# Performance work log

Hardware: AMD Instinct MI355X
Metric: run time of the kernel (lower is better)

## Reference

```python
import jax, jax.numpy as jnp
import numpy as np

CONF_THRES = 0.8   # from module constant
NMS_THRES = 0.4    # from module constant
PERSON_ID = 0      # COCO 'person' is class index 0 in coco.names
IMG_SIZE = 416.0
TOPK = 4096        # static cap on post-threshold candidates (>= expected survivors)


def setup_inputs() -> dict:
    key = jax.random.key(0)
    B, N, C = 8, 10647, 85  # YOLOv3@416: (13^2+26^2+52^2)*3 anchors, 4+1+80 channels
    det = jax.random.uniform(key, (B, N, C), dtype=jnp.float32)
    # scale xywh columns to pixel coordinates; obj/class confs stay in [0,1]
    scale = jnp.concatenate([jnp.full((4,), IMG_SIZE, jnp.float32),
                             jnp.ones((C - 4,), jnp.float32)])
    return {"detections": det * scale}


def _xywh2xyxy(b):
    x, y, w, h = b[..., 0], b[..., 1], b[..., 2], b[..., 3]
    return jnp.stack([x - w / 2, y - h / 2, x + w / 2, y + h / 2], axis=-1)


def _iou_matrix(boxes):
    # boxes [K,4] xyxy; matches torch-yolov3 bbox_iou (+1 pixel convention, 1e-16 eps)
    x1, y1, x2, y2 = boxes[:, 0], boxes[:, 1], boxes[:, 2], boxes[:, 3]
    iw = jnp.clip(jnp.minimum(x2[:, None], x2[None, :]) - jnp.maximum(x1[:, None], x1[None, :]) + 1, 0)
    ih = jnp.clip(jnp.minimum(y2[:, None], y2[None, :]) - jnp.maximum(y1[:, None], y1[None, :]) + 1, 0)
    inter = iw * ih
    area = (x2 - x1 + 1) * (y2 - y1 + 1)
    return inter / (area[:, None] + area[None, :] - inter + 1e-16)


def _nms_image(det):
    # det [N,85]: greedy class-aware NMS identical in keep-set to the torch loop
    obj = det[:, 4]
    cls_conf = jnp.max(det[:, 5:], axis=-1)
    cls_pred = jnp.argmax(det[:, 5:], axis=-1)
    valid = obj >= CONF_THRES
    # torch sorts candidates by obj_conf * max class conf, descending
    score = jnp.where(valid, obj * cls_conf, -jnp.inf)
    _, idx = jax.lax.top_k(score, TOPK)
    boxes = _xywh2xyxy(det[idx, :4])
    cc = cls_conf[idx]
    cp = cls_pred[idx]
    v = valid[idx]
    overlap = (_iou_matrix(boxes) > NMS_THRES) & (cp[:, None] == cp[None, :])
    upper = jnp.arange(TOPK)[None, :] > jnp.arange(TOPK)[:, None]  # only suppress later boxes

    def body(i, supp):
        alive = (~supp[i]) & v[i]
        return supp | (overlap[i] & upper[i] & alive)

    supp = jax.lax.fori_loop(0, TOPK, body, jnp.zeros((TOPK,), bool))
    keep = v & ~supp
    # _extract_results: class-conf probs sorted descending per image
    probs = jnp.where(keep, cc, 0.0)
    probs = jnp.flip(jnp.sort(probs), axis=-1)
    # image contributes only if 'person' detected (CATEGORY_NAME check)
    is_ok = jnp.any(keep & (cp == PERSON_ID))
    return probs * is_ok.astype(probs.dtype)


def reference(detections):
    # [B, TOPK] padded prob matrix; rows without a kept 'person' box are zeroed
    return jax.vmap(_nms_image)(detections)
```

## Files before the change

### kernel.cpp

```cpp
#include <hip/hip_runtime.h>


#define NCH    85
#define NCLS   80
#define TOPK   4096
#define CAP    96
#define KBLK   64
#define RWAVES 8

__device__ __forceinline__ float rlf(float v, int l) {
    return __uint_as_float(__builtin_amdgcn_readlane(__float_as_uint(v), l));
}
__device__ __forceinline__ int rli(int v, int l) {
    return __builtin_amdgcn_readlane(v, l);
}

__global__ void score_kernel(const float* __restrict__ det,
                             float2* __restrict__ A,
                             unsigned char* __restrict__ Cc,
                             float4* __restrict__ REC,
                             int N, int NP, int total) {
#pragma clang fp contract(off)
    int w    = (blockIdx.x * blockDim.x + threadIdx.x) >> 6;
    int lane = threadIdx.x & 63;
    if (w >= total) return;
    const float* row = det + (size_t)w * NCH;
    int b = w / N, i = w - b * N;

    float obj = row[4];
    if (obj < 0.8f) {
        if (lane == 0) Cc[(size_t)b * NP + i] = 0xFFu;
        return;
    }
    float va = row[lane];
    float vb = (lane < NCH - 64) ? row[64 + lane] : -1.0f;
    float bestv = -1.0f; int bestc = 1 << 30;
    if (lane >= 5) { bestv = va; bestc = lane - 5; }
    if (lane < NCH - 64) {
        int c2 = 59 + lane;
        if (vb > bestv || (vb == bestv && c2 < bestc)) { bestv = vb; bestc = c2; }
    }
    for (int m = 32; m >= 1; m >>= 1) {
        float ov = __shfl_xor(bestv, m);
        int   oc = __shfl_xor(bestc, m);
        if (ov > bestv || (ov == bestv && oc < bestc)) { bestv = ov; bestc = oc; }
    }
    float x  = rlf(va, 0), y  = rlf(va, 1);
    float bw = rlf(va, 2), bh = rlf(va, 3);
    if (lane == 0) {
        float hw = bw * 0.5f, hh = bh * 0.5f;
        A[(size_t)b * NP + i]  = make_float2(obj * bestv, bestv);
        Cc[(size_t)b * NP + i] = (unsigned char)bestc;
        REC[(size_t)w] = make_float4(x - hw, y - hh, x + hw, y + hh);
    }
}

__global__ void __launch_bounds__(64) nms_kernel(
        const float2* __restrict__ A,
        const unsigned char* __restrict__ Cc,
        const float4* __restrict__ REC,
        float* __restrict__ kv,
        int*   __restrict__ kcnt,
        int N, int NT, int NP) {
#pragma clang fp contract(off)
    int cell = blockIdx.x;
    int b = cell / NCLS, c = cell % NCLS;
    int lane = threadIdx.x;
    unsigned long long mlt = (1ull << lane) - 1ull;

    __shared__ int lidx[CAP];
    __shared__ int tmpidx[CAP];

    const unsigned char* Cb = Cc + (size_t)b * NP;
    int cnt = 0;
    uint4 q = *(const uint4*)(Cb + lane * 16);
    for (int t = 0; t < NT; t++) {
        uint4 qn;
        if (t + 1 < NT) qn = *(const uint4*)(Cb + (size_t)(t + 1) * 1024 + lane * 16);
        int i0 = t * 1024 + lane * 16;
        unsigned xs[4] = { q.x, q.y, q.z, q.w };
        unsigned mm = 0;
        #pragma unroll
        for (int kk = 0; kk < 16; kk++) {
            unsigned byte = (xs[kk >> 2] >> ((kk & 3) * 8)) & 0xFFu;
            if (byte == (unsigned)c && (i0 + kk) < N) mm |= 1u << kk;
        }
        if (__ballot(mm != 0)) {
            #pragma unroll
            for (int kk = 0; kk < 16; kk++) {
                unsigned long long mk = __ballot((mm >> kk) & 1u);
                if (mk) {
                    if ((mm >> kk) & 1u) {
                        int p = cnt + __popcll(mk & mlt);
                        if (p < CAP) lidx[p] = i0 + kk;
                    }
                    cnt += __popcll(mk);
                }
            }
        }
        q = qn;
    }
    int n = cnt < CAP ? cnt : CAP;
    if (n == 0) { if (lane == 0) kcnt[cell] = 0; return; }

    bool a0 = lane < n, a1 = lane + 64 < n;
    const float2* Ab = A + (size_t)b * NP;
    int id0 = a0 ? lidx[lane]      : 0;
    int id1 = a1 ? lidx[lane + 64] : 0;
    float s0 = a0 ? Ab[id0].x : 0.0f;
    float s1 = a1 ? Ab[id1].x : 0.0f;

    int r0 = 0, r1 = 0;
    int m0 = n < 64 ? n : 64;
    for (int j = 0; j < m0; j++) {
        float sj = rlf(s0, j); int ij = rli(id0, j);
        r0 += (sj > s0) || (sj == s0 && ij < id0);
        r1 += (sj > s1) || (sj == s1 && ij < id1);
    }
    for (int j = 64; j < n; j++) {
        float sj = rlf(s1, j - 64); int ij = rli(id1, j - 64);
        r0 += (sj > s0) || (sj == s0 && ij < id0);
        r1 += (sj > s1) || (sj == s1 && ij < id1);
    }
    if (a0) tmpidx[r0] = id0;
    if (a1) tmpidx[r1] = id1;
    int di0 = a0 ? tmpidx[lane]      : 0;
    int di1 = a1 ? tmpidx[lane + 64] : 0;

    float scc = 0, x10 = 0, y10 = 0, x20 = 0, y20 = 0, ar0 = 0;
    if (a0) {
        scc = Ab[di0].y;
        float4 rc = REC[(size_t)b * N + di0];
        x10 = rc.x; y10 = rc.y; x20 = rc.z; y20 = rc.w;
        ar0 = (x20 - x10 + 1.0f) * (y20 - y10 + 1.0f);
    }
    float tcc = 0, x11 = 0, y11 = 0, x21 = 0, y21 = 0, ar1 = 0;
    if (a1) {
        tcc = Ab[di1].y;
        float4 rc = REC[(size_t)b * N + di1];
        x11 = rc.x; y11 = rc.y; x21 = rc.z; y21 = rc.w;
        ar1 = (x21 - x11 + 1.0f) * (y21 - y11 + 1.0f);
    }

    unsigned long long col0 = 0, col1a = 0, col1b = 0;
    for (int i = 0; i < n; i++) {
        float ix1, iy1, ix2, iy2, iar;
        if (i < 64) {
            ix1 = rlf(x10, i); iy1 = rlf(y10, i);
            ix2 = rlf(x20, i); iy2 = rlf(y20, i); iar = rlf(ar0, i);
        } else {
            ix1 = rlf(x11, i - 64); iy1 = rlf(y11, i - 64);
            ix2 = rlf(x21, i - 64); iy2 = rlf(y21, i - 64); iar = rlf(ar1, i - 64);
        }
        if (lane > i && lane < n) {
            float iw = fminf(ix2, x20) - fmaxf(ix1, x10) + 1.0f;
            float ih = fminf(iy2, y20) - fmaxf(iy1, y10) + 1.0f;
            iw = fmaxf(iw, 0.0f); ih = fmaxf(ih, 0.0f);
            float inter = iw * ih;
            float iou = inter / (iar + ar0 - inter + 1e-16f);
            if (iou > 0.4f) col0 |= 1ull << i;
        }
        if (n > 64) {
            int j2 = lane + 64;
            if (j2 > i && j2 < n) {
                float iw = fminf(ix2, x21) - fmaxf(ix1, x11) + 1.0f;
                float ih = fminf(iy2, y21) - fmaxf(iy1, y11) + 1.0f;
                iw = fmaxf(iw, 0.0f); ih = fmaxf(ih, 0.0f);
                float inter = iw * ih;
                float iou = inter / (iar + ar1 - inter + 1e-16f);
                if (iou > 0.4f) {
                    if (i < 64) col1a |= 1ull << i;
                    else        col1b |= 1ull << (i - 64);
                }
            }
        }
    }

    bool sup0 = false, sup1 = false;
    for (int ii = 0; ii < n; ii++) {
        bool alive;
        if (ii < 64) alive = !((__ballot(sup0) >> ii) & 1ull);
        else         alive = !((__ballot(sup1) >> (ii - 64)) & 1ull);
        if (alive) {
            if (ii < 64) {
                sup0 = sup0 | (((col0  >> ii) & 1ull) != 0);
                sup1 = sup1 | (((col1a >> ii) & 1ull) != 0);
            } else {
                sup1 = sup1 | (((col1b >> (ii - 64)) & 1ull) != 0);
            }
        }
    }

    unsigned long long alive0 = __ballot((!sup0) && a0);
    int kn0 = __popcll(alive0);
    unsigned long long alive1 = (n > 64) ? __ballot((!sup1) && a1) : 0ull;
    int kn = kn0 + __popcll(alive1);
    float* kvc = kv + (size_t)cell * CAP;
    if ((!sup0) && a0) kvc[__popcll(alive0 & mlt)] = scc;
    if ((!sup1) && a1) kvc[kn0 + __popcll(alive1 & mlt)] = tcc;
    if (lane == 0) kcnt[cell] = kn;
}

__global__ void __launch_bounds__(512) rank_out_kernel(
        const float* __restrict__ kv,
        const int*   __restrict__ kcnt,
        float* __restrict__ out) {
    int b     = blockIdx.x / KBLK;
    int chunk = blockIdx.x % KBLK;
    int tid   = threadIdx.x;
    int lane  = tid & 63;
    int wid   = tid >> 6;
    int i     = chunk * 64 + lane;

    __shared__ int   off[NCLS];
    __shared__ float v[TOPK] __attribute__((aligned(16)));
    __shared__ int   part[RWAVES][64];

    if (tid < NCLS) off[tid] = kcnt[b * NCLS + tid];
    __syncthreads();
    #pragma unroll
    for (int s = 1; s < NCLS; s <<= 1) {
        int x = 0;
        if (tid < NCLS && tid >= s) x = off[tid - s];
        __syncthreads();
        if (tid < NCLS) off[tid] += x;
        __syncthreads();
    }
    int cnt = off[NCLS - 1];
    if (cnt > TOPK) cnt = TOPK;
    float f = (off[0] > 0) ? 1.0f : 0.0f;

    if (chunk * 64 >= cnt) {
        if (wid == 0) out[(size_t)b * TOPK + i] = 0.0f;
        return;
    }

    for (int cell = wid; cell < NCLS; cell += RWAVES) {
        int e1 = off[cell];
        int e0 = (cell == 0) ? 0 : off[cell - 1];
        int kc = e1 - e0;
        const float* src = kv + (size_t)(b * NCLS + cell) * CAP;
        for (int j = lane; j < kc; j += 64)
            if (e0 + j < TOPK) v[e0 + j] = src[j];
    }
    __syncthreads();

    float val = (i < cnt) ? v[i] : 0.0f;
    int seg = (cnt + RWAVES - 1) / RWAVES;
    int j0 = wid * seg;
    int j1 = j0 + seg; if (j1 > cnt) j1 = cnt;

    int r = 0, j = j0;
    for (; j < j1 && (j & 3); j++) {
        float t = v[j]; r += (t > val) || (t == val && j < i);
    }
    for (; j + 4 <= j1; j += 4) {
        float4 q = *(const float4*)&v[j];
        r += (q.x > val) || (q.x == val && (j + 0) < i);
        r += (q.y > val) || (q.y == val && (j + 1) < i);
        r += (q.z > val) || (q.z == val && (j + 2) < i);
        r += (q.w > val) || (q.w == val && (j + 3) < i);
    }
    for (; j < j1; j++) {
        float t = v[j]; r += (t > val) || (t == val && j < i);
    }
    part[wid][lane] = r;
    __syncthreads();

    if (wid == 0) {
        if (i < cnt) {
            int rank = 0;
            #pragma unroll
            for (int qq = 0; qq < RWAVES; qq++) rank += part[qq][lane];
            out[(size_t)b * TOPK + rank] = val * f;
        } else {
            out[(size_t)b * TOPK + i] = 0.0f;
        }
    }
}

extern "C" void kernel_launch(void* const* d_in, const int* in_sizes, int n_in,
                              void* d_out, int out_size, void* d_ws, size_t ws_size,
                              hipStream_t stream) {
    const float* det = (const float*)d_in[0];
    float* out = (float*)d_out;

    int B = out_size / TOPK;
    int N = in_sizes[0] / (B * NCH);
    int total = B * N;
    int NT = (N + 1023) / 1024;
    int NP = NT * 1024;

    char* p = (char*)d_ws;
    auto align256 = [](size_t x) { return (x + 255) & ~(size_t)255; };
    size_t o = 0;
    unsigned char* Cc = (unsigned char*)(p + o); o = align256(o + (size_t)B * NP);
    float2* A   = (float2*)(p + o);              o = align256(o + (size_t)B * NP * sizeof(float2));
    float4* REC = (float4*)(p + o);              o = align256(o + (size_t)total * sizeof(float4));
    float*  kv  = (float*)(p + o);               o = align256(o + (size_t)B * NCLS * CAP * sizeof(float));
    int*   kcnt = (int*)(p + o);

    int gridA = (total + 3) / 4;
    score_kernel<<<gridA, 256, 0, stream>>>(det, A, Cc, REC, N, NP, total);
    nms_kernel<<<B * NCLS, 64, 0, stream>>>(A, Cc, REC, kv, kcnt, N, NT, NP);
    rank_out_kernel<<<B * KBLK, 512, 0, stream>>>(kv, kcnt, out);
}
```

Baseline: 62.18 us.

## Fuse NMS and rank-output kernels via per-image atomic completion counters

Result: slower. 115.0 us (+85.0%).

```diff
diff --git a/kernel.cpp b/kernel.cpp
--- a/kernel.cpp
+++ b/kernel.cpp
@@ -7,6 +7,8 @@
 #define CAP    96
 #define KBLK   64
 #define RWAVES 8
+#define PBB    80
+#define BPI    10
 
 __device__ __forceinline__ float rlf(float v, int l) {
     return __uint_as_float(__builtin_amdgcn_readlane(__float_as_uint(v), l));
@@ -19,8 +21,11 @@
                              float2* __restrict__ A,
                              unsigned char* __restrict__ Cc,
                              float4* __restrict__ REC,
+                             int* __restrict__ done,
                              int N, int NP, int total) {
 #pragma clang fp contract(off)
+    if (blockIdx.x == 0 && threadIdx.x < 16) done[threadIdx.x] = 0;
+
     int w    = (blockIdx.x * blockDim.x + threadIdx.x) >> 6;
     int lane = threadIdx.x & 63;
     if (w >= total) return;
@@ -55,166 +60,178 @@
     }
 }
 
-__global__ void __launch_bounds__(64) nms_kernel(
+__global__ void __launch_bounds__(512, 4) fused_kernel(
         const float2* __restrict__ A,
         const unsigned char* __restrict__ Cc,
         const float4* __restrict__ REC,
         float* __restrict__ kv,
         int*   __restrict__ kcnt,
+        int*   __restrict__ done,
+        float* __restrict__ out,
         int N, int NT, int NP) {
 #pragma clang fp contract(off)
-    int cell = blockIdx.x;
-    int b = cell / NCLS, c = cell % NCLS;
-    int lane = threadIdx.x;
-    unsigned long long mlt = (1ull << lane) - 1ull;
-
-    __shared__ int lidx[CAP];
-    __shared__ int tmpidx[CAP];
-
-    const unsigned char* Cb = Cc + (size_t)b * NP;
-    int cnt = 0;
-    uint4 q = *(const uint4*)(Cb + lane * 16);
-    for (int t = 0; t < NT; t++) {
-        uint4 qn;
-        if (t + 1 < NT) qn = *(const uint4*)(Cb + (size_t)(t + 1) * 1024 + lane * 16);
-        int i0 = t * 1024 + lane * 16;
-        unsigned xs[4] = { q.x, q.y, q.z, q.w };
-        unsigned mm = 0;
-        #pragma unroll
-        for (int kk = 0; kk < 16; kk++) {
-            unsigned byte = (xs[kk >> 2] >> ((kk & 3) * 8)) & 0xFFu;
-            if (byte == (unsigned)c && (i0 + kk) < N) mm |= 1u << kk;
-        }
-        if (__ballot(mm != 0)) {
-            #pragma unroll
-            for (int kk = 0; kk < 16; kk++) {
-                unsigned long long mk = __ballot((mm >> kk) & 1u);
-                if (mk) {
-                    if ((mm >> kk) & 1u) {
-                        int p = cnt + __popcll(mk & mlt);
-                        if (p < CAP) lidx[p] = i0 + kk;
-                    }
-                    cnt += __popcll(mk);
-                }
-            }
-        }
-        q = qn;
-    }
-    int n = cnt < CAP ? cnt : CAP;
-    if (n == 0) { if (lane == 0) kcnt[cell] = 0; return; }
-
-    bool a0 = lane < n, a1 = lane + 64 < n;
-    const float2* Ab = A + (size_t)b * NP;
-    int id0 = a0 ? lidx[lane]      : 0;
-    int id1 = a1 ? lidx[lane + 64] : 0;
-    float s0 = a0 ? Ab[id0].x : 0.0f;
-    float s1 = a1 ? Ab[id1].x : 0.0f;
-
-    int r0 = 0, r1 = 0;
-    int m0 = n < 64 ? n : 64;
-    for (int j = 0; j < m0; j++) {
-        float sj = rlf(s0, j); int ij = rli(id0, j);
-        r0 += (sj > s0) || (sj == s0 && ij < id0);
-        r1 += (sj > s1) || (sj == s1 && ij < id1);
-    }
-    for (int j = 64; j < n; j++) {
-        float sj = rlf(s1, j - 64); int ij = rli(id1, j - 64);
-        r0 += (sj > s0) || (sj == s0 && ij < id0);
-        r1 += (sj > s1) || (sj == s1 && ij < id1);
-    }
-    if (a0) tmpidx[r0] = id0;
-    if (a1) tmpidx[r1] = id1;
-    int di0 = a0 ? tmpidx[lane]      : 0;
-    int di1 = a1 ? tmpidx[lane + 64] : 0;
-
-    float scc = 0, x10 = 0, y10 = 0, x20 = 0, y20 = 0, ar0 = 0;
-    if (a0) {
-        scc = Ab[di0].y;
-        float4 rc = REC[(size_t)b * N + di0];
-        x10 = rc.x; y10 = rc.y; x20 = rc.z; y20 = rc.w;
-        ar0 = (x20 - x10 + 1.0f) * (y20 - y10 + 1.0f);
-    }
-    float tcc = 0, x11 = 0, y11 = 0, x21 = 0, y21 = 0, ar1 = 0;
-    if (a1) {
-        tcc = Ab[di1].y;
-        float4 rc = REC[(size_t)b * N + di1];
-        x11 = rc.x; y11 = rc.y; x21 = rc.z; y21 = rc.w;
-        ar1 = (x21 - x11 + 1.0f) * (y21 - y11 + 1.0f);
-    }
-
-    unsigned long long col0 = 0, col1a = 0, col1b = 0;
-    for (int i = 0; i < n; i++) {
-        float ix1, iy1, ix2, iy2, iar;
-        if (i < 64) {
-            ix1 = rlf(x10, i); iy1 = rlf(y10, i);
-            ix2 = rlf(x20, i); iy2 = rlf(y20, i); iar = rlf(ar0, i);
-        } else {
-            ix1 = rlf(x11, i - 64); iy1 = rlf(y11, i - 64);
-            ix2 = rlf(x21, i - 64); iy2 = rlf(y21, i - 64); iar = rlf(ar1, i - 64);
-        }
-        if (lane > i && lane < n) {
-            float iw = fminf(ix2, x20) - fmaxf(ix1, x10) + 1.0f;
-            float ih = fminf(iy2, y20) - fmaxf(iy1, y10) + 1.0f;
-            iw = fmaxf(iw, 0.0f); ih = fmaxf(ih, 0.0f);
-            float inter = iw * ih;
-            float iou = inter / (iar + ar0 - inter + 1e-16f);
-            if (iou > 0.4f) col0 |= 1ull << i;
-        }
-        if (n > 64) {
-            int j2 = lane + 64;
-            if (j2 > i && j2 < n) {
-                float iw = fminf(ix2, x21) - fmaxf(ix1, x11) + 1.0f;
-                float ih = fminf(iy2, y21) - fmaxf(iy1, y11) + 1.0f;
-                iw = fmaxf(iw, 0.0f); ih = fmaxf(ih, 0.0f);
-                float inter = iw * ih;
-                float iou = inter / (iar + ar1 - inter + 1e-16f);
-                if (iou > 0.4f) {
-                    if (i < 64) col1a |= 1ull << i;
-                    else        col1b |= 1ull << (i - 64);
-                }
-            }
-        }
-    }
-
-    bool sup0 = false, sup1 = false;
-    for (int ii = 0; ii < n; ii++) {
-        bool alive;
-        if (ii < 64) alive = !((__ballot(sup0) >> ii) & 1ull);
-        else         alive = !((__ballot(sup1) >> (ii - 64)) & 1ull);
-        if (alive) {
-            if (ii < 64) {
-                sup0 = sup0 | (((col0  >> ii) & 1ull) != 0);
-                sup1 = sup1 | (((col1a >> ii) & 1ull) != 0);
-            } else {
-                sup1 = sup1 | (((col1b >> (ii - 64)) & 1ull) != 0);
-            }
-        }
-    }
-
-    unsigned long long alive0 = __ballot((!sup0) && a0);
-    int kn0 = __popcll(alive0);
-    unsigned long long alive1 = (n > 64) ? __ballot((!sup1) && a1) : 0ull;
-    int kn = kn0 + __popcll(alive1);
-    float* kvc = kv + (size_t)cell * CAP;
-    if ((!sup0) && a0) kvc[__popcll(alive0 & mlt)] = scc;
-    if ((!sup1) && a1) kvc[kn0 + __popcll(alive1 & mlt)] = tcc;
-    if (lane == 0) kcnt[cell] = kn;
-}
-
-__global__ void __launch_bounds__(512) rank_out_kernel(
-        const float* __restrict__ kv,
-        const int*   __restrict__ kcnt,
-        float* __restrict__ out) {
-    int b     = blockIdx.x / KBLK;
-    int chunk = blockIdx.x % KBLK;
-    int tid   = threadIdx.x;
-    int lane  = tid & 63;
-    int wid   = tid >> 6;
-    int i     = chunk * 64 + lane;
-
+    const int bid  = blockIdx.x;
+    const int tid  = threadIdx.x;
+    const int lane = tid & 63;
+    const int wid  = tid >> 6;
+
+    __shared__ int   lidx[8][CAP];
+    __shared__ int   tmp2[8][CAP];
     __shared__ int   off[NCLS];
     __shared__ float v[TOPK] __attribute__((aligned(16)));
     __shared__ int   part[RWAVES][64];
+
+    if (bid < PBB) {
+        int cell = bid * 8 + wid;
+        int b = cell / NCLS, c = cell % NCLS;
+        unsigned long long mlt = (1ull << lane) - 1ull;
+
+        const unsigned char* Cb = Cc + (size_t)b * NP;
+        int cnt = 0;
+        uint4 q = *(const uint4*)(Cb + lane * 16);
+        for (int t = 0; t < NT; t++) {
+            uint4 qn;
+            if (t + 1 < NT) qn = *(const uint4*)(Cb + (size_t)(t + 1) * 1024 + lane * 16);
+            int i0 = t * 1024 + lane * 16;
+            unsigned xs[4] = { q.x, q.y, q.z, q.w };
+            unsigned mm = 0;
+            #pragma unroll
+            for (int kk = 0; kk < 16; kk++) {
+                unsigned byte = (xs[kk >> 2] >> ((kk & 3) * 8)) & 0xFFu;
+                if (byte == (unsigned)c && (i0 + kk) < N) mm |= 1u << kk;
+            }
+            if (__ballot(mm != 0)) {
+                #pragma unroll
+                for (int kk = 0; kk < 16; kk++) {
+                    unsigned long long mk = __ballot((mm >> kk) & 1u);
+                    if (mk) {
+                        if ((mm >> kk) & 1u) {
+                            int p = cnt + __popcll(mk & mlt);
+                            if (p < CAP) lidx[wid][p] = i0 + kk;
+                        }
+                        cnt += __popcll(mk);
+                    }
+                }
+            }
+            q = qn;
+        }
+        int n = cnt < CAP ? cnt : CAP;
+        if (n == 0) {
+            if (lane == 0) kcnt[cell] = 0;
+        } else {
+            bool a0 = lane < n, a1 = lane + 64 < n;
+            const float2* Ab = A + (size_t)b * NP;
+            int id0 = a0 ? lidx[wid][lane]      : 0;
+            int id1 = a1 ? lidx[wid][lane + 64] : 0;
+            float s0 = a0 ? Ab[id0].x : 0.0f;
+            float s1 = a1 ? Ab[id1].x : 0.0f;
+
+            int r0 = 0, r1 = 0;
+            int m0 = n < 64 ? n : 64;
+            for (int j = 0; j < m0; j++) {
+                float sj = rlf(s0, j); int ij = rli(id0, j);
+                r0 += (sj > s0) || (sj == s0 && ij < id0);
+                r1 += (sj > s1) || (sj == s1 && ij < id1);
+            }
+            for (int j = 64; j < n; j++) {
+                float sj = rlf(s1, j - 64); int ij = rli(id1, j - 64);
+                r0 += (sj > s0) || (sj == s0 && ij < id0);
+                r1 += (sj > s1) || (sj == s1 && ij < id1);
+            }
+            if (a0) tmp2[wid][r0] = id0;
+            if (a1) tmp2[wid][r1] = id1;
+            int di0 = a0 ? tmp2[wid][lane]      : 0;
+            int di1 = a1 ? tmp2[wid][lane + 64] : 0;
+
+            float scc = 0, x10 = 0, y10 = 0, x20 = 0, y20 = 0, ar0 = 0;
+            if (a0) {
+                scc = Ab[di0].y;
+                float4 rc = REC[(size_t)b * N + di0];
+                x10 = rc.x; y10 = rc.y; x20 = rc.z; y20 = rc.w;
+                ar0 = (x20 - x10 + 1.0f) * (y20 - y10 + 1.0f);
+            }
+            float tcc = 0, x11 = 0, y11 = 0, x21 = 0, y21 = 0, ar1 = 0;
+            if (a1) {
+                tcc = Ab[di1].y;
+                float4 rc = REC[(size_t)b * N + di1];
+                x11 = rc.x; y11 = rc.y; x21 = rc.z; y21 = rc.w;
+                ar1 = (x21 - x11 + 1.0f) * (y21 - y11 + 1.0f);
+            }
+
+            unsigned long long col0 = 0, col1a = 0, col1b = 0;
+            for (int i = 0; i < n; i++) {
+                float ix1, iy1, ix2, iy2, iar;
+                if (i < 64) {
+                    ix1 = rlf(x10, i); iy1 = rlf(y10, i);
+                    ix2 = rlf(x20, i); iy2 = rlf(y20, i); iar = rlf(ar0, i);
+                } else {
+                    ix1 = rlf(x11, i - 64); iy1 = rlf(y11, i - 64);
+                    ix2 = rlf(x21, i - 64); iy2 = rlf(y21, i - 64); iar = rlf(ar1, i - 64);
+                }
+                if (lane > i && lane < n) {
+                    float iw = fminf(ix2, x20) - fmaxf(ix1, x10) + 1.0f;
+                    float ih = fminf(iy2, y20) - fmaxf(iy1, y10) + 1.0f;
+                    iw = fmaxf(iw, 0.0f); ih = fmaxf(ih, 0.0f);
+                    float inter = iw * ih;
+                    float iou = inter / (iar + ar0 - inter + 1e-16f);
+                    if (iou > 0.4f) col0 |= 1ull << i;
+                }
+                if (n > 64) {
+                    int j2 = lane + 64;
+                    if (j2 > i && j2 < n) {
+                        float iw = fminf(ix2, x21) - fmaxf(ix1, x11) + 1.0f;
+                        float ih = fminf(iy2, y21) - fmaxf(iy1, y11) + 1.0f;
+                        iw = fmaxf(iw, 0.0f); ih = fmaxf(ih, 0.0f);
+                        float inter = iw * ih;
+                        float iou = inter / (iar + ar1 - inter + 1e-16f);
+                        if (iou > 0.4f) {
+                            if (i < 64) col1a |= 1ull << i;
+                            else        col1b |= 1ull << (i - 64);
+                        }
+                    }
+                }
+            }
+
+            bool sup0 = false, sup1 = false;
+            for (int ii = 0; ii < n; ii++) {
+                bool alive;
+                if (ii < 64) alive = !((__ballot(sup0) >> ii) & 1ull);
+                else         alive = !((__ballot(sup1) >> (ii - 64)) & 1ull);
+                if (alive) {
+                    if (ii < 64) {
+                        sup0 = sup0 | (((col0  >> ii) & 1ull) != 0);
+                        sup1 = sup1 | (((col1a >> ii) & 1ull) != 0);
+                    } else {
+                        sup1 = sup1 | (((col1b >> (ii - 64)) & 1ull) != 0);
+                    }
+                }
+            }
+
+            unsigned long long alive0 = __ballot((!sup0) && a0);
+            int kn0 = __popcll(alive0);
+            unsigned long long alive1 = (n > 64) ? __ballot((!sup1) && a1) : 0ull;
+            int kn = kn0 + __popcll(alive1);
+            float* kvc = kv + (size_t)cell * CAP;
+            if ((!sup0) && a0) kvc[__popcll(alive0 & mlt)] = scc;
+            if ((!sup1) && a1) kvc[kn0 + __popcll(alive1 & mlt)] = tcc;
+            if (lane == 0) kcnt[cell] = kn;
+        }
+        __syncthreads();
+        if (tid == 0)
+            __hip_atomic_fetch_add(&done[bid / BPI], 1,
+                                   __ATOMIC_RELEASE, __HIP_MEMORY_SCOPE_AGENT);
+    }
+
+    int b     = bid / KBLK;
+    int chunk = bid % KBLK;
+    int i     = chunk * 64 + lane;
+
+    if (tid == 0) {
+        while (__hip_atomic_load(&done[b], __ATOMIC_ACQUIRE,
+                                 __HIP_MEMORY_SCOPE_AGENT) < BPI)
+            __builtin_amdgcn_s_sleep(8);
+    }
+    __syncthreads();
 
     if (tid < NCLS) off[tid] = kcnt[b * NCLS + tid];
     __syncthreads();
@@ -298,10 +315,15 @@
     float2* A   = (float2*)(p + o);              o = align256(o + (size_t)B * NP * sizeof(float2));
     float4* REC = (float4*)(p + o);              o = align256(o + (size_t)total * sizeof(float4));
     float*  kv  = (float*)(p + o);               o = align256(o + (size_t)B * NCLS * CAP * sizeof(float));
-    int*   kcnt = (int*)(p + o);
+    int*   kcnt = (int*)(p + o);                 o = align256(o + (size_t)B * NCLS * sizeof(int));
+    int*   done = (int*)(p + o);
 
     int gridA = (total + 3) / 4;
-    score_kernel<<<gridA, 256, 0, stream>>>(det, A, Cc, REC, N, NP, total);
-    nms_kernel<<<B * NCLS, 64, 0, stream>>>(A, Cc, REC, kv, kcnt, N, NT, NP);
-    rank_out_kernel<<<B * KBLK, 512, 0, stream>>>(kv, kcnt, out);
-}
+    score_kernel<<<gridA, 256, 0, stream>>>(det, A, Cc, REC, done, N, NP, total);
+
+    void* args[] = { (void*)&A, (void*)&Cc, (void*)&REC, (void*)&kv,
+                     (void*)&kcnt, (void*)&done, (void*)&out,
+                     (void*)&N, (void*)&NT, (void*)&NP };
+    hipLaunchCooperativeKernel((void*)fused_kernel, dim3(B * KBLK), dim3(512),
+                               args, 0, stream);
+}
```
